# Performance work log

Measured on AMD Instinct MI355X. Metric: run time of the kernel, lower is better.

Reference implementation:

```python
import jax, jax.numpy as jnp
import numpy as np

D_MODEL = 512

def setup_inputs() -> dict:
    key = jax.random.key(0)
    k1, k2, k3 = jax.random.split(key, 3)
    B, N1, N2 = 16, 2048, 2048
    x1 = jax.random.normal(k1, (B, N1, D_MODEL), dtype=jnp.float32)
    x2 = jax.random.normal(k2, (B, N2, D_MODEL), dtype=jnp.float32)
    node_mask = jnp.ones((B, N1), dtype=jnp.bool_)
    # learned parameter: q_proj weight, stored torch-style [out, in]
    Wq = jax.random.normal(k3, (D_MODEL, D_MODEL), dtype=jnp.float32) * (1.0 / np.sqrt(D_MODEL))
    return {"x1": x1, "x2": x2, "node_mask": node_mask, "Wq": Wq}


def reference(x1, x2, node_mask, Wq):
    # Q = x1 @ Wq^T   (torch Linear with weight [out, in], no bias)
    Q = jnp.einsum('bnd,ed->bne', x1, Wq)            # [B, N1, 512]
    D = x2                                            # [B, N2, 512]
    # similarity matrix L = Q @ D^T
    L = jnp.einsum('bnd,bmd->bnm', Q, D)              # [B, N1, N2]
    # attention over document axis (dim=2)
    A_D = jax.nn.softmax(L, axis=2)                   # [B, N1, N2]
    # C_D = Q^T @ A_D -> transposed to [B, N2, 512]
    C_D = jnp.einsum('bnd,bnm->bmd', Q, A_D)          # [B, N2, 512]
    # attention over query axis (dim=1), then transposed: A_Q [B, N2, N1]
    A_Q = jnp.swapaxes(jax.nn.softmax(L, axis=1), 1, 2)
    # C_Q = D^T @ A_Q -> transposed to [B, N1, 512]
    C_Q = jnp.einsum('bmd,bmn->bnd', D, A_Q)          # [B, N1, 512]
    return (C_Q, C_D, A_D, A_Q)
```

## Files before the change

kernel.cpp:

```cpp
#include <hip/hip_runtime.h>

namespace {

constexpr int Bn = 16;
constexpr int Nn = 2048;
constexpr int Dn = 512;

typedef _Float16 h4 __attribute__((ext_vector_type(4)));
typedef _Float16 h8 __attribute__((ext_vector_type(8)));
typedef float    fx4 __attribute__((ext_vector_type(4)));

__device__ __forceinline__ void gld16(const _Float16* g, _Float16* l) {
  typedef const void __attribute__((address_space(1))) gvoid;
  typedef void __attribute__((address_space(3))) lvoid;
  __builtin_amdgcn_global_load_lds((gvoid*)g, (lvoid*)l, 16, 0, 0);
}

__device__ __forceinline__ void stage_gld(const _Float16* __restrict__ g, int ld,
    int r0, int k0, _Float16* __restrict__ lds, int t)
{
  #pragma unroll
  for (int i = 0; i < 2; ++i) {
    int chunk = i*256 + t;
    gld16(g + (long)(r0 + (chunk >> 2))*ld + k0 + (chunk & 3)*8, lds + chunk*8);
  }
}

__device__ __forceinline__ void load_f32(const float* __restrict__ g, int ld,
    int r0, int k0, int t, fx4* regs)
{
  #pragma unroll
  for (int rd = 0; rd < 4; ++rd)
    regs[rd] = *(const fx4*)(g + (long)(r0 + rd*32 + (t >> 3))*ld + k0 + (t & 7)*4);
}
template<int S>
__device__ __forceinline__ void write_cvt(const fx4* regs, _Float16* __restrict__ lds, int t)
{
  const int c = (t & 7)*4;
  #pragma unroll
  for (int rd = 0; rd < 4; ++rd) {
    int r = rd*32 + (t >> 3);
    h4 o;
    #pragma unroll
    for (int i = 0; i < 4; ++i) o[i] = (_Float16)regs[rd][i];
    *(h4*)(lds + r*S + c) = o;
  }
}

struct RegsA3 { h8 v0, v1; fx4 k00, k01, k10, k11; };
__device__ __forceinline__ void load_A3(const _Float16* __restrict__ g, int ld,
    int r0, int k0, int t, const float* __restrict__ kofs, RegsA3& R)
{
  {
    int chunk = t, r = chunk >> 2, c = (chunk & 3)*8;
    R.v0  = *(const h8*)(g + (long)(r0 + r)*ld + k0 + c);
    R.k00 = *(const fx4*)(kofs + k0 + c);
    R.k01 = *(const fx4*)(kofs + k0 + c + 4);
  }
  {
    int chunk = 256 + t, r = chunk >> 2, c = (chunk & 3)*8;
    R.v1  = *(const h8*)(g + (long)(r0 + r)*ld + k0 + c);
    R.k10 = *(const fx4*)(kofs + k0 + c);
    R.k11 = *(const fx4*)(kofs + k0 + c + 4);
  }
}
template<int S>
__device__ __forceinline__ void write_A3(const RegsA3& R, _Float16* __restrict__ lds, int t)
{
  {
    int chunk = t, r = chunk >> 2, c = (chunk & 3)*8;
    h8 o;
    #pragma unroll
    for (int j = 0; j < 4; ++j) {
      o[j]   = (_Float16)__expf((float)R.v0[j]   - R.k00[j]);
      o[4+j] = (_Float16)__expf((float)R.v0[4+j] - R.k01[j]);
    }
    *(h8*)(lds + r*S + c) = o;
  }
  {
    int chunk = 256 + t, r = chunk >> 2, c = (chunk & 3)*8;
    h8 o;
    #pragma unroll
    for (int j = 0; j < 4; ++j) {
      o[j]   = (_Float16)__expf((float)R.v1[j]   - R.k10[j]);
      o[4+j] = (_Float16)__expf((float)R.v1[4+j] - R.k11[j]);
    }
    *(h8*)(lds + r*S + c) = o;
  }
}

template<int MA, int MB, int EPI, int TY>
__global__ __launch_bounds__(256) void gemm128(
    const void* __restrict__ Ap, long sA,
    const void* __restrict__ Bp, long sB,
    void* __restrict__ Cp, long sC, int ldc,
    void* __restrict__ C2p, long sC2, int ldc2,
    int lda, int ldb, int K,
    const float* __restrict__ kofs,
    float* __restrict__ rowPM, float* __restrict__ rowPS,
    float* __restrict__ colPM, float* __restrict__ colPS)
{
  constexpr int SA = (MA == 0) ? 32 : 40;
  constexpr int SB = (MB == 0) ? 32 : 40;
  constexpr int ASZ = 128*SA, BSZ = 128*SB;
  constexpr int DB = 2*ASZ + 2*BSZ;
  constexpr int SMEM = (EPI >= 1 && DB < 128*136) ? 128*136 : DB;
  __shared__ _Float16 smem[SMEM];

  constexpr int TILES = 16*TY;
  const int bid = blockIdx.x;
  const int xcd = bid & 7, slot = bid >> 3;
  const int b = xcd*2 + slot/TILES;
  const int tile = slot % TILES;
  const int by = tile % TY, bx = tile / TY;
  const int row0 = bx*128, col0 = by*128;

  const int t = threadIdx.x, w = t >> 6, l = t & 63;
  const int wr = w >> 1, wc = w & 1, l15 = l & 15, lg = l >> 4;

  const void* Ab;
  const void* Bb;
  if constexpr (MA == 1) Ab = (const void*)((const float*)Ap + (long)b*sA);
  else                   Ab = (const void*)((const _Float16*)Ap + (long)b*sA);
  if constexpr (MB == 1) Bb = (const void*)((const float*)Bp + (long)b*sB);
  else                   Bb = (const void*)((const _Float16*)Bp + (long)b*sB);

  const float* ko = nullptr;
  if constexpr (MA == 3) ko = kofs + (long)b*Nn;

  fx4 acc[4][4];
  #pragma unroll
  for (int fi = 0; fi < 4; ++fi)
    #pragma unroll
    for (int fj = 0; fj < 4; ++fj)
      acc[fi][fj] = (fx4){0.f, 0.f, 0.f, 0.f};

  const int NT = K/32;
  fx4 regA[4], regB[4];
  RegsA3 rA3;

  if constexpr (MA == 0)      stage_gld((const _Float16*)Ab, lda, row0, 0, smem, t);
  else if constexpr (MA == 1) load_f32((const float*)Ab, lda, row0, 0, t, regA);
  else                        load_A3((const _Float16*)Ab, lda, row0, 0, t, ko, rA3);
  if constexpr (MB == 0)      stage_gld((const _Float16*)Bb, ldb, col0, 0, smem + 2*ASZ, t);
  else                        load_f32((const float*)Bb, ldb, col0, 0, t, regB);
  if constexpr (MA == 1)      write_cvt<SA>(regA, smem, t);
  if constexpr (MA == 3)      write_A3<SA>(rA3, smem, t);
  if constexpr (MB == 1)      write_cvt<SB>(regB, smem + 2*ASZ, t);
  __syncthreads();

  for (int kt = 0; kt < NT; ++kt) {
    const int cur = kt & 1, nxt = cur ^ 1;
    const int k1 = (kt + 1)*32;
    _Float16* cA = smem + cur*ASZ;
    _Float16* cB = smem + 2*ASZ + cur*BSZ;
    _Float16* nA = smem + nxt*ASZ;
    _Float16* nB = smem + 2*ASZ + nxt*BSZ;

    if (kt + 1 < NT) {
      if constexpr (MA == 0)      stage_gld((const _Float16*)Ab, lda, row0, k1, nA, t);
      else if constexpr (MA == 1) load_f32((const float*)Ab, lda, row0, k1, t, regA);
      else                        load_A3((const _Float16*)Ab, lda, row0, k1, t, ko, rA3);
      if constexpr (MB == 0)      stage_gld((const _Float16*)Bb, ldb, col0, k1, nB, t);
      else                        load_f32((const float*)Bb, ldb, col0, k1, t, regB);
    }

    h8 af[4], bf[4];
    #pragma unroll
    for (int fi = 0; fi < 4; ++fi)
      af[fi] = *(const h8*)(cA + (wr*64 + fi*16 + l15)*SA + lg*8);
    #pragma unroll
    for (int fj = 0; fj < 4; ++fj)
      bf[fj] = *(const h8*)(cB + (wc*64 + fj*16 + l15)*SB + lg*8);
    #pragma unroll
    for (int fi = 0; fi < 4; ++fi)
      #pragma unroll
      for (int fj = 0; fj < 4; ++fj)
        acc[fi][fj] = __builtin_amdgcn_mfma_f32_16x16x32_f16(af[fi], bf[fj], acc[fi][fj], 0, 0, 0);

    if (kt + 1 < NT) {
      if constexpr (MA == 1) write_cvt<SA>(regA, nA, t);
      if constexpr (MA == 3) write_A3<SA>(rA3, nA, t);
      if constexpr (MB == 1) write_cvt<SB>(regB, nB, t);
    }
    __syncthreads();
  }

  if constexpr (EPI == 0) {
    float* Cb = (float*)Cp + (long)b*sC;
    #pragma unroll
    for (int fi = 0; fi < 4; ++fi)
      #pragma unroll
      for (int fj = 0; fj < 4; ++fj)
        #pragma unroll
        for (int j = 0; j < 4; ++j)
          Cb[(long)(row0 + wr*64 + fi*16 + lg*4 + j)*ldc + col0 + wc*64 + fj*16 + l15] = acc[fi][fj][j];
  }

  if constexpr (EPI >= 1) {
    if constexpr (EPI == 1) {
      #pragma unroll
      for (int fi = 0; fi < 4; ++fi)
        #pragma unroll
        for (int fj = 0; fj < 4; ++fj)
          #pragma unroll
          for (int j = 0; j < 4; ++j)
            acc[fi][fj][j] = (float)(_Float16)acc[fi][fj][j];
    }

    #pragma unroll
    for (int fi = 0; fi < 4; ++fi) {
      #pragma unroll
      for (int j = 0; j < 4; ++j) {
        int rr = wr*64 + fi*16 + lg*4 + j;
        int key = (rr >> 3) & 7;
        #pragma unroll
        for (int fj = 0; fj < 4; ++fj) {
          int cc = wc*64 + fj*16 + l15;
          smem[rr*136 + ((((cc >> 3) ^ key) << 3) | (cc & 7))] = (_Float16)acc[fi][fj][j];
        }
      }
    }
    __syncthreads();
    _Float16* Cb  = (_Float16*)Cp  + (long)b*sC;
    _Float16* C2b = (_Float16*)C2p + (long)b*sC2;
    #pragma unroll
    for (int rd = 0; rd < 8; ++rd) {
      int r = rd*16 + (t >> 4);
      int g = (t & 15) ^ ((r >> 3) & 7);
      h8 v = *(const h8*)(smem + r*136 + g*8);
      *(h8*)(Cb + (long)(row0 + r)*ldc + col0 + (t & 15)*8) = v;
    }
    {
      const int q = t & 15, keyq = q & 7, n8 = q*8;
      #pragma unroll
      for (int rd = 0; rd < 8; ++rd) {
        int dl = rd*16 + (t >> 4);
        int gbase = ((dl >> 3) ^ keyq) << 3, c7 = dl & 7;
        h8 v;
        #pragma unroll
        for (int i = 0; i < 8; ++i)
          v[i] = smem[(n8 + i)*136 + gbase + c7];
        *(h8*)(C2b + (long)(col0 + dl)*ldc2 + row0 + n8) = v;
      }
    }
  }

  if constexpr (EPI == 1) {
    float rm[4][4], rs[4][4];
    #pragma unroll
    for (int fi = 0; fi < 4; ++fi)
      #pragma unroll
      for (int j = 0; j < 4; ++j)
        rm[fi][j] = fmaxf(fmaxf(acc[fi][0][j], acc[fi][1][j]),
                          fmaxf(acc[fi][2][j], acc[fi][3][j]));
    #pragma unroll
    for (int m = 1; m < 16; m <<= 1)
      #pragma unroll
      for (int fi = 0; fi < 4; ++fi)
        #pragma unroll
        for (int j = 0; j < 4; ++j)
          rm[fi][j] = fmaxf(rm[fi][j], __shfl_xor(rm[fi][j], m, 64));
    #pragma unroll
    for (int fi = 0; fi < 4; ++fi)
      #pragma unroll
      for (int j = 0; j < 4; ++j) {
        float s = 0.f;
        #pragma unroll
        for (int fj = 0; fj < 4; ++fj)
          s += __expf(acc[fi][fj][j] - rm[fi][j]);
        rs[fi][j] = s;
      }
    #pragma unroll
    for (int m = 1; m < 16; m <<= 1)
      #pragma unroll
      for (int fi = 0; fi < 4; ++fi)
        #pragma unroll
        for (int j = 0; j < 4; ++j)
          rs[fi][j] += __shfl_xor(rs[fi][j], m, 64);
    if (l15 == 0) {
      #pragma unroll
      for (int fi = 0; fi < 4; ++fi)
        #pragma unroll
        for (int j = 0; j < 4; ++j) {
          int row = row0 + wr*64 + fi*16 + lg*4 + j;
          long idx = ((long)b*Nn + row)*32 + by*2 + wc;
          rowPM[idx] = rm[fi][j];
          rowPS[idx] = rs[fi][j];
        }
    }
    float cm[4], cs[4];
    #pragma unroll
    for (int fj = 0; fj < 4; ++fj) {
      float v = -3.4e38f;
      #pragma unroll
      for (int fi = 0; fi < 4; ++fi)
        #pragma unroll
        for (int j = 0; j < 4; ++j)
          v = fmaxf(v, acc[fi][fj][j]);
      cm[fj] = v;
    }
    #pragma unroll
    for (int fj = 0; fj < 4; ++fj) {
      cm[fj] = fmaxf(cm[fj], __shfl_xor(cm[fj], 16, 64));
      cm[fj] = fmaxf(cm[fj], __shfl_xor(cm[fj], 32, 64));
    }
    #pragma unroll
    for (int fj = 0; fj < 4; ++fj) {
      float s = 0.f;
      #pragma unroll
      for (int fi = 0; fi < 4; ++fi)
        #pragma unroll
        for (int j = 0; j < 4; ++j)
          s += __expf(acc[fi][fj][j] - cm[fj]);
      cs[fj] = s;
    }
    #pragma unroll
    for (int fj = 0; fj < 4; ++fj) {
      cs[fj] += __shfl_xor(cs[fj], 16, 64);
      cs[fj] += __shfl_xor(cs[fj], 32, 64);
    }
    if (l < 16) {
      #pragma unroll
      for (int fj = 0; fj < 4; ++fj) {
        int col = col0 + wc*64 + fj*16 + l15;
        long idx = ((long)b*Nn + col)*32 + bx*2 + wr;
        colPM[idx] = cm[fj];
        colPS[idx] = cs[fj];
      }
    }
  }
}

__global__ __launch_bounds__(256) void convert_x2(const float* __restrict__ x2,
    _Float16* __restrict__ x2h, _Float16* __restrict__ x2hT)
{
  __shared__ _Float16 lt[64*66];
  const int b = blockIdx.z, m0 = blockIdx.x*64, d0 = blockIdx.y*64;
  const int t = threadIdx.x;
  const float* xb = x2 + (long)b*Nn*Dn;
  _Float16* hb = x2h + (long)b*Nn*Dn;
  #pragma unroll
  for (int rd = 0; rd < 4; ++rd) {
    int r = rd*16 + (t >> 4), c = (t & 15)*4;
    fx4 v = *(const fx4*)(xb + (long)(m0 + r)*Dn + d0 + c);
    h4 h;
    #pragma unroll
    for (int i = 0; i < 4; ++i) { h[i] = (_Float16)v[i]; lt[r*66 + c + i] = h[i]; }
    *(h4*)(hb + (long)(m0 + r)*Dn + d0 + c) = h;
  }
  __syncthreads();
  _Float16* tb = x2hT + (long)b*Dn*Nn;
  #pragma unroll
  for (int rd = 0; rd < 4; ++rd) {
    int dl = rd*16 + (t >> 4), ml = (t & 15)*4;
    h4 h;
    #pragma unroll
    for (int i = 0; i < 4; ++i) h[i] = lt[(ml + i)*66 + dl];
    *(h4*)(tb + (long)(d0 + dl)*Nn + m0 + ml) = h;
  }
}

__global__ __launch_bounds__(256) void reduce_stats(
    const float* __restrict__ rowPM, const float* __restrict__ rowPS,
    const float* __restrict__ colPM, const float* __restrict__ colPS,
    float* __restrict__ rofs, float* __restrict__ cofs)
{
  const int w = threadIdx.x >> 6, l = threadIdx.x & 63;
  const long row = (long)blockIdx.x*4 + w;
  const float* PM = blockIdx.y ? colPM : rowPM;
  const float* PS = blockIdx.y ? colPS : rowPS;
  float m0 = PM[row*32 + (l & 31)];
  float s0 = PS[row*32 + (l & 31)];
  float m = m0;
  #pragma unroll
  for (int k = 1; k < 32; k <<= 1) m = fmaxf(m, __shfl_xor(m, k, 64));
  float v = s0 * __expf(m0 - m);
  #pragma unroll
  for (int k = 1; k < 32; k <<= 1) v += __shfl_xor(v, k, 64);
  if (l == 0) {
    float ofs = m + __logf(v);
    if (blockIdx.y == 0) rofs[row] = ofs;
    else                 cofs[row] = ofs;
  }
}

__global__ __launch_bounds__(256) void finalize_AQ(const _Float16* __restrict__ Lh,
    float* __restrict__ AD, float* __restrict__ AQ,
    const float* __restrict__ rofs, const float* __restrict__ cofs)
{
  __shared__ float l2[64*65];
  const int b = blockIdx.z, n0 = blockIdx.x*64, m0 = blockIdx.y*64;
  const int t = threadIdx.x;
  const _Float16* Lb = Lh + (long)b*Nn*Nn;
  float* Db = AD + (long)b*Nn*Nn;
  #pragma unroll
  for (int rd = 0; rd < 4; ++rd) {
    int r = rd*16 + (t >> 4), c = (t & 15)*4;
    h4 v = *(const h4*)(Lb + (long)(n0 + r)*Nn + m0 + c);
    float ro = rofs[(long)b*Nn + n0 + r];
    fx4 co = *(const fx4*)(cofs + (long)b*Nn + m0 + c);
    fx4 e1;
    #pragma unroll
    for (int i = 0; i < 4; ++i) {
      float lv = (float)v[i];
      e1[i] = __expf(lv - ro);
      l2[r*65 + c + i] = __expf(lv - co[i]);
    }
    *(fx4*)(Db + (long)(n0 + r)*Nn + m0 + c) = e1;
  }
  __syncthreads();
  float* Qb = AQ + (long)b*Nn*Nn;
  #pragma unroll
  for (int rd = 0; rd < 4; ++rd) {
    int ml = rd*16 + (t >> 4), nl = (t & 15)*4;
    fx4 q;
    #pragma unroll
    for (int i = 0; i < 4; ++i) q[i] = l2[(nl + i)*65 + ml];
    *(fx4*)(Qb + (long)(m0 + ml)*Nn + n0 + nl) = q;
  }
}

}

extern "C" void kernel_launch(void* const* d_in, const int* in_sizes, int n_in,
                              void* d_out, int out_size, void* d_ws, size_t ws_size,
                              hipStream_t stream)
{
  const float* x1 = (const float*)d_in[0];
  const float* x2 = (const float*)d_in[1];
  const float* Wq = (const float*)d_in[3];

  float* out = (float*)d_out;
  float* C_Q = out;
  float* C_D = out + (long)Bn*Nn*Dn;
  float* A_D = out + 2L*Bn*Nn*Dn;
  float* A_Q = A_D + (long)Bn*Nn*Nn;

  char* ws = (char*)d_ws;
  _Float16* Qh   = (_Float16*)ws;
  _Float16* QhT  = Qh   + (long)Bn*Nn*Dn;
  _Float16* x2h  = QhT  + (long)Bn*Dn*Nn;
  _Float16* x2hT = x2h  + (long)Bn*Nn*Dn;
  _Float16* Lh   = x2hT + (long)Bn*Dn*Nn;
  float* rofs = (float*)(Lh + (long)Bn*Nn*Nn);
  float* cofs = rofs + (long)Bn*Nn;

  _Float16* Lt = (_Float16*)A_Q;
  float* rowPM = (float*)((char*)A_Q + sizeof(_Float16)*(long)Bn*Nn*Nn);
  float* rowPS = rowPM + (long)Bn*Nn*32;
  float* colPM = rowPS + (long)Bn*Nn*32;
  float* colPS = colPM + (long)Bn*Nn*32;

  dim3 blk(256);

  convert_x2<<<dim3(32, 8, 16), blk, 0, stream>>>(x2, x2h, x2hT);

  gemm128<1,1,2,4><<<dim3(1024), blk, 0, stream>>>(
      x1, (long)Nn*Dn, Wq, 0L,
      Qh, (long)Nn*Dn, Dn, QhT, (long)Dn*Nn, Nn,
      Dn, Dn, Dn,
      nullptr, nullptr, nullptr, nullptr, nullptr);

  gemm128<0,0,1,16><<<dim3(4096), blk, 0, stream>>>(
      Qh, (long)Nn*Dn, x2h, (long)Nn*Dn,
      Lh, (long)Nn*Nn, Nn, Lt, (long)Nn*Nn, Nn,
      Dn, Dn, Dn,
      nullptr, rowPM, rowPS, colPM, colPS);

  reduce_stats<<<dim3(Bn*Nn/4, 2), blk, 0, stream>>>(rowPM, rowPS, colPM, colPS, rofs, cofs);

  gemm128<3,0,0,4><<<dim3(1024), blk, 0, stream>>>(
      Lh, (long)Nn*Nn, x2hT, (long)Dn*Nn,
      C_Q, (long)Nn*Dn, Dn, nullptr, 0L, 0,
      Nn, Nn, Nn,
      cofs, nullptr, nullptr, nullptr, nullptr);

  gemm128<3,0,0,4><<<dim3(1024), blk, 0, stream>>>(
      Lt, (long)Nn*Nn, QhT, (long)Dn*Nn,
      C_D, (long)Nn*Dn, Dn, nullptr, 0L, 0,
      Nn, Nn, Nn,
      rofs, nullptr, nullptr, nullptr, nullptr);

  finalize_AQ<<<dim3(32, 32, 16), blk, 0, stream>>>(Lh, A_D, A_Q, rofs, cofs);
}
```

Measured before the change: 630.8 us.

## Use dedicated 128x256-tile kernel for the two exp-weighted context GEMMs

Replaces the generic 128x128 gemm128 instantiation for C_Q and C_D with a specialised kernel that uses 128x256 output tiles (4x8 MFMA fragments per wave), halving the grid to 512 blocks. An XCD-aware block-to-batch mapping keeps each batch's work on one XCD. The wider tile halves how many times the exp-weighted A operand (the large N×N matrix) is re-read and converted, at the cost of more accumulator registers and only 512 blocks, which may reduce occupancy.

```diff
diff --git a/kernel.cpp b/kernel.cpp
--- a/kernel.cpp
+++ b/kernel.cpp
@@ -21,6 +21,16 @@
 {
   #pragma unroll
   for (int i = 0; i < 2; ++i) {
+    int chunk = i*256 + t;
+    gld16(g + (long)(r0 + (chunk >> 2))*ld + k0 + (chunk & 3)*8, lds + chunk*8);
+  }
+}
+
+__device__ __forceinline__ void stage_gld256(const _Float16* __restrict__ g, int ld,
+    int r0, int k0, _Float16* __restrict__ lds, int t)
+{
+  #pragma unroll
+  for (int i = 0; i < 4; ++i) {
     int chunk = i*256 + t;
     gld16(g + (long)(r0 + (chunk >> 2))*ld + k0 + (chunk & 3)*8, lds + chunk*8);
   }
@@ -332,6 +342,85 @@
   }
 }
 
+__global__ __launch_bounds__(256, 2) void gemm_expw(
+    const _Float16* __restrict__ Ap, const _Float16* __restrict__ Bp,
+    float* __restrict__ Cp, const float* __restrict__ kofs)
+{
+  constexpr int SA = 40;
+  constexpr int ASZ = 128*SA;
+  constexpr int BSZ = 256*32;
+  __shared__ _Float16 smem[2*ASZ + 2*BSZ];
+
+  const int bid = blockIdx.x;
+  const int xcd = bid & 7, slot = bid >> 3;
+  const int b = xcd*2 + (slot >> 5);
+  const int tile = slot & 31;
+  const int by = tile & 1, bx = tile >> 1;
+  const int row0 = bx*128, col0 = by*256;
+
+  const int t = threadIdx.x, w = t >> 6, l = t & 63;
+  const int wr = w >> 1, wc = w & 1, l15 = l & 15, lg = l >> 4;
+
+  const _Float16* Ab = Ap + (long)b*Nn*Nn;
+  const _Float16* Bb = Bp + (long)b*Dn*Nn;
+  const float* ko = kofs + (long)b*Nn;
+
+  fx4 acc[4][8];
+  #pragma unroll
+  for (int fi = 0; fi < 4; ++fi)
+    #pragma unroll
+    for (int fj = 0; fj < 8; ++fj)
+      acc[fi][fj] = (fx4){0.f, 0.f, 0.f, 0.f};
+
+  const int NT = Nn/32;
+  RegsA3 rA3;
+
+  load_A3(Ab, Nn, row0, 0, t, ko, rA3);
+  stage_gld256(Bb, Nn, col0, 0, smem + 2*ASZ, t);
+  write_A3<SA>(rA3, smem, t);
+  __syncthreads();
+
+  for (int kt = 0; kt < NT; ++kt) {
+    const int cur = kt & 1, nxt = cur ^ 1;
+    const int k1 = (kt + 1)*32;
+    _Float16* cA = smem + cur*ASZ;
+    _Float16* cB = smem + 2*ASZ + cur*BSZ;
+    _Float16* nA = smem + nxt*ASZ;
+    _Float16* nB = smem + 2*ASZ + nxt*BSZ;
+
+    if (kt + 1 < NT) {
+      load_A3(Ab, Nn, row0, k1, t, ko, rA3);
+      stage_gld256(Bb, Nn, col0, k1, nB, t);
+    }
+
+    h8 af[4], bf[8];
+    #pragma unroll
+    for (int fi = 0; fi < 4; ++fi)
+      af[fi] = *(const h8*)(cA + (wr*64 + fi*16 + l15)*SA + lg*8);
+    #pragma unroll
+    for (int fj = 0; fj < 8; ++fj)
+      bf[fj] = *(const h8*)(cB + (wc*128 + fj*16 + l15)*32 + lg*8);
+    #pragma unroll
+    for (int fi = 0; fi < 4; ++fi)
+      #pragma unroll
+      for (int fj = 0; fj < 8; ++fj)
+        acc[fi][fj] = __builtin_amdgcn_mfma_f32_16x16x32_f16(af[fi], bf[fj], acc[fi][fj], 0, 0, 0);
+
+    if (kt + 1 < NT)
+      write_A3<SA>(rA3, nA, t);
+    __syncthreads();
+  }
+
+  float* Cb = Cp + (long)b*Nn*Dn;
+  #pragma unroll
+  for (int fi = 0; fi < 4; ++fi)
+    #pragma unroll
+    for (int fj = 0; fj < 8; ++fj)
+      #pragma unroll
+      for (int j = 0; j < 4; ++j)
+        Cb[(long)(row0 + wr*64 + fi*16 + lg*4 + j)*Dn + col0 + wc*128 + fj*16 + l15] = acc[fi][fj][j];
+}
+
 __global__ __launch_bounds__(256) void convert_x2(const float* __restrict__ x2,
     _Float16* __restrict__ x2h, _Float16* __restrict__ x2hT)
 {
@@ -470,17 +559,9 @@
 
   reduce_stats<<<dim3(Bn*Nn/4, 2), blk, 0, stream>>>(rowPM, rowPS, colPM, colPS, rofs, cofs);
 
-  gemm128<3,0,0,4><<<dim3(1024), blk, 0, stream>>>(
-      Lh, (long)Nn*Nn, x2hT, (long)Dn*Nn,
-      C_Q, (long)Nn*Dn, Dn, nullptr, 0L, 0,
-      Nn, Nn, Nn,
-      cofs, nullptr, nullptr, nullptr, nullptr);
-
-  gemm128<3,0,0,4><<<dim3(1024), blk, 0, stream>>>(
-      Lt, (long)Nn*Nn, QhT, (long)Dn*Nn,
-      C_D, (long)Nn*Dn, Dn, nullptr, 0L, 0,
-      Nn, Nn, Nn,
-      rofs, nullptr, nullptr, nullptr, nullptr);
+  gemm_expw<<<dim3(512), blk, 0, stream>>>(Lh, x2hT, C_Q, cofs);
+
+  gemm_expw<<<dim3(512), blk, 0, stream>>>(Lt, QhT, C_D, rofs);
 
   finalize_AQ<<<dim3(32, 32, 16), blk, 0, stream>>>(Lh, A_D, A_Q, rofs, cofs);
 }
```

Measured after the change: 623.5 us. No clear change (-1.2%).
